# Performance work log

Measured on AMD Instinct MI355X. Metric: run time of the kernel, lower is better.

## Reference

```python
import jax, jax.numpy as jnp
import numpy as np

B, S, D = 2, 2048, 1024
E, K, DFF = 8, 2, 4 * 1024
EPS_GATE = 1e-8
EPS_LN = 1e-5


def setup_inputs() -> dict:
    key = jax.random.key(0)
    ks = jax.random.split(key, 4)
    scaled = lambda k, shape, fan: (jax.random.normal(k, shape, jnp.float32) / np.sqrt(fan).astype(np.float32))
    return {
        "x": jax.random.normal(ks[0], (B, S, D), jnp.float32),
        "Wg": scaled(ks[1], (D, E), D),
        "bg": jnp.zeros((E,), jnp.float32),
        "W1": scaled(ks[2], (E, D, DFF), D),
        "b1": jnp.zeros((E, DFF), jnp.float32),
        "W2": scaled(ks[3], (E, DFF, D), DFF),
        "b2": jnp.zeros((E, D), jnp.float32),
        "gamma": jnp.ones((D,), jnp.float32),
        "beta": jnp.zeros((D,), jnp.float32),
    }


def reference(x, Wg, bg, W1, b1, W2, b2, gamma, beta):
    b, s, d = x.shape
    xf = x.reshape(-1, d)                       # [T, D]
    T = xf.shape[0]
    num_experts = Wg.shape[1]

    # Gating: softmax over experts, top-k, renormalize selected weights.
    logits = xf @ Wg + bg                       # [T, E]
    w = jax.nn.softmax(logits, axis=-1)
    top_w, top_idx = jax.lax.top_k(w, K)        # [T, K]
    top_w = top_w / (top_w.sum(axis=-1, keepdims=True) + EPS_GATE)

    # Dense combine weights: cw[t, e] = renormalized weight if e selected else 0.
    cw = jnp.zeros((T, num_experts), xf.dtype).at[
        jnp.arange(T)[:, None], top_idx].add(top_w)

    # Expert FFNs (loop over small fixed expert count), weighted combine.
    out = jnp.zeros_like(xf)
    for e in range(num_experts):
        h = jax.nn.gelu(xf @ W1[e] + b1[e], approximate=False)  # [T, DFF]
        y = h @ W2[e] + b2[e]                                    # [T, D]
        out = out + cw[:, e:e + 1] * y

    # LayerNorm over the whole combined output (as in the torch module).
    mu = out.mean(axis=-1, keepdims=True)
    var = out.var(axis=-1, keepdims=True)
    out = (out - mu) / jnp.sqrt(var + EPS_LN) * gamma + beta
    return out.reshape(b, s, d)
```

## Files before the change

### kernel.cpp

```cpp
#include <hip/hip_runtime.h>
#include <hip/hip_bf16.h>

#define TOK  4096
#define DIMD 1024
#define NEXP 8
#define DFFN 4096
#define NSLOT   (TOK*2 + NEXP*128)
#define NRB128  ((TOK*2)/128 + NEXP)

typedef __attribute__((ext_vector_type(8))) short bf16x8;
typedef __attribute__((ext_vector_type(4))) float f32x4;

__device__ __forceinline__ unsigned short f2bf(float f){
  unsigned int u = __float_as_uint(f);
  unsigned int r = u + 0x7FFFu + ((u >> 16) & 1u);
  return (unsigned short)(r >> 16);
}

__device__ __forceinline__ float bf2f(unsigned short h){
  unsigned int u = ((unsigned int)h) << 16;
  return __uint_as_float(u);
}

__device__ __forceinline__ void gload_lds16(const void* g, void* l){
  __builtin_amdgcn_global_load_lds(
      (const __attribute__((address_space(1))) unsigned int*)g,
      (__attribute__((address_space(3))) unsigned int*)l, 16, 0, 0);
}

__global__ __launch_bounds__(256) void k_tr(
    const float* __restrict__ W1, unsigned short* __restrict__ w1t,
    const float* __restrict__ W2, unsigned short* __restrict__ w2t)
{
  int bid = blockIdx.x;
  const float* I; unsigned short* O; int R, C, r0, c0;
  if (bid < 2048){
    const int e = bid >> 8, rem = bid & 255;
    R = DIMD; C = DFFN;
    I = W1 + (size_t)e * R * C; O = w1t + (size_t)e * R * C;
    r0 = (rem >> 5) * 128; c0 = (rem & 31) * 128;
  } else {
    bid -= 2048;
    const int e = bid >> 8, rem = bid & 255;
    R = DFFN; C = DIMD;
    I = W2 + (size_t)e * R * C; O = w2t + (size_t)e * R * C;
    r0 = (rem >> 3) * 128; c0 = (rem & 7) * 128;
  }
  __shared__ alignas(16) unsigned short tile[128*128];
  const int tid = threadIdx.x;
  const int qw = tid & 31;
  const int rw = tid >> 5;
  float4 v[16];
  #pragma unroll
  for (int it = 0; it < 16; ++it){
    const int r = it * 8 + rw;
    v[it] = *(const float4*)(I + (size_t)(r0 + r) * C + c0 + qw * 4);
  }
  #pragma unroll
  for (int it = 0; it < 16; ++it){
    const int r = it * 8 + rw;
    ushort4 o;
    o.x = f2bf(v[it].x); o.y = f2bf(v[it].y); o.z = f2bf(v[it].z); o.w = f2bf(v[it].w);
    const int slot = qw ^ ((r >> 2) & 31);
    *(ushort4*)&tile[r * 128 + slot * 4] = o;
  }
  __syncthreads();
  const int p  = tid & 31;
  const int cb = tid >> 5;
  #pragma unroll
  for (int it = 0; it < 4; ++it){
    const int cg = cb * 4 + it;
    const int sl = (cg ^ p) * 4;
    const ushort4 a0 = *(const ushort4*)&tile[(4*p + 0) * 128 + sl];
    const ushort4 a1 = *(const ushort4*)&tile[(4*p + 1) * 128 + sl];
    const ushort4 a2 = *(const ushort4*)&tile[(4*p + 2) * 128 + sl];
    const ushort4 a3 = *(const ushort4*)&tile[(4*p + 3) * 128 + sl];
    ushort4 o;
    o.x = a0.x; o.y = a1.x; o.z = a2.x; o.w = a3.x;
    *(ushort4*)(O + (size_t)(c0 + 4*cg + 0) * R + r0 + 4*p) = o;
    o.x = a0.y; o.y = a1.y; o.z = a2.y; o.w = a3.y;
    *(ushort4*)(O + (size_t)(c0 + 4*cg + 1) * R + r0 + 4*p) = o;
    o.x = a0.z; o.y = a1.z; o.z = a2.z; o.w = a3.z;
    *(ushort4*)(O + (size_t)(c0 + 4*cg + 2) * R + r0 + 4*p) = o;
    o.x = a0.w; o.y = a1.w; o.z = a2.w; o.w = a3.w;
    *(ushort4*)(O + (size_t)(c0 + 4*cg + 3) * R + r0 + 4*p) = o;
  }
}

__global__ __launch_bounds__(256) void k_gate(
    const float* __restrict__ x, const float* __restrict__ Wg,
    const float* __restrict__ bg, int* __restrict__ topidx,
    float* __restrict__ topw, int* __restrict__ pos, int* __restrict__ count,
    unsigned short* __restrict__ xb)
{
  const int gb = blockIdx.x;
  const int wid = threadIdx.x >> 6, lane = threadIdx.x & 63;
  const int t = gb * 4 + wid;
  const float* xr = x + (size_t)t * DIMD;
  unsigned short* xbr = xb + (size_t)t * DIMD;
  float acc[NEXP] = {0.f,0.f,0.f,0.f,0.f,0.f,0.f,0.f};
  #pragma unroll
  for (int j = 0; j < DIMD/64; ++j){
    const int d = j*64 + lane;
    const float xv = xr[d];
    xbr[d] = f2bf(xv);
    const float4 wa = *(const float4*)(Wg + (size_t)d*NEXP);
    const float4 wb = *(const float4*)(Wg + (size_t)d*NEXP + 4);
    acc[0] += xv*wa.x; acc[1] += xv*wa.y; acc[2] += xv*wa.z; acc[3] += xv*wa.w;
    acc[4] += xv*wb.x; acc[5] += xv*wb.y; acc[6] += xv*wb.z; acc[7] += xv*wb.w;
  }
  #pragma unroll
  for (int e = 0; e < NEXP; ++e){
    float v = acc[e];
    #pragma unroll
    for (int o = 32; o > 0; o >>= 1) v += __shfl_xor(v, o);
    acc[e] = v;
  }
  if (lane == 0){
    float lg[NEXP], m = -1e30f;
    #pragma unroll
    for (int e = 0; e < NEXP; ++e){ lg[e] = acc[e] + bg[e]; m = fmaxf(m, lg[e]); }
    float p[NEXP], S = 0.f;
    #pragma unroll
    for (int e = 0; e < NEXP; ++e){ p[e] = expf(lg[e] - m); S += p[e]; }
    int e0 = 0;
    #pragma unroll
    for (int e = 1; e < NEXP; ++e) if (p[e] > p[e0]) e0 = e;
    int e1 = (e0 == 0) ? 1 : 0;
    #pragma unroll
    for (int e = 0; e < NEXP; ++e){
      if (e == e0 || e == e1) continue;
      if (p[e] > p[e1]) e1 = e;
    }
    const float denom = p[e0] + p[e1] + 1e-8f * S;
    const float w0 = p[e0] / denom, w1 = p[e1] / denom;
    const int p0 = atomicAdd(&count[e0], 1);
    const int p1 = atomicAdd(&count[e1], 1);
    topidx[t*2] = e0; topidx[t*2+1] = e1;
    topw[t*2] = w0;   topw[t*2+1] = w1;
    pos[t*2] = p0;    pos[t*2+1] = p1;
  }
}

__global__ __launch_bounds__(256) void k_scatter(
    const int* __restrict__ topidx, const int* __restrict__ pos,
    const int* __restrict__ count, int* __restrict__ slot_of, int* __restrict__ tok_of)
{
  int basee[NEXP]; int bacc = 0;
  #pragma unroll
  for (int q = 0; q < NEXP; ++q){
    basee[q] = bacc << 7;
    bacc += (count[q] + 127) >> 7;
  }
  const int t = blockIdx.x * 256 + threadIdx.x;
  #pragma unroll
  for (int k = 0; k < 2; ++k){
    const int e = topidx[t*2+k];
    const int g = basee[e] + pos[t*2+k];
    slot_of[t*2+k] = g;
    tok_of[g] = t;
  }
}

template<int KD, int KSLICES, int NT, int MODE, int WAVES, int BM, int BN, int MINW>
__global__ __launch_bounds__(WAVES*64, MINW) void k_gemm(
    const unsigned short* __restrict__ A, const unsigned short* __restrict__ Bt,
    const float* __restrict__ bias, const int* __restrict__ tok_of,
    const int* __restrict__ count,
    unsigned short* __restrict__ outH, unsigned short* __restrict__ outY,
    unsigned short* __restrict__ outY1)
{
  const int by = blockIdx.y;
  int e = -1, b0 = 0;
  #pragma unroll
  for (int q = 0; q < NEXP; ++q){
    const int nb = (count[q] + 127) >> 7;
    if (e < 0){ if (by < b0 + nb) e = q; else b0 += nb; }
  }
  if (e < 0) return;
  const int ct = blockIdx.x;
  const int ks = (KSLICES == 1) ? 0 : blockIdx.z;
  constexpr int KSL = KD / KSLICES;
  const int kbase = ks * KSL;
  const int row0 = by * 128;
  constexpr int T   = WAVES * 64;
  constexpr int RA  = BM*8 / T;
  constexpr int RB  = BN*8 / T;
  constexpr int WN  = BN / 64;
  constexpr int WM  = WAVES / WN;
  constexpr int MR  = BM / WM / 16;
  __shared__ alignas(16) unsigned short sA[BM*64];
  __shared__ alignas(16) unsigned short sB[BN*64];
  const int tid = threadIdx.x, wid = tid >> 6, lane = tid & 63;

  const unsigned short* aptr[RA];
  #pragma unroll
  for (int i = 0; i < RA; ++i){
    const int s = i*T + tid;
    const int row = s >> 3;
    const int c = (s & 7) ^ (row & 7);
    size_t arow;
    if (MODE == 1) arow = (size_t)tok_of[row0 + row] * KD;
    else           arow = (size_t)(row0 + row) * KD;
    aptr[i] = A + arow + kbase + c*8;
  }
  const unsigned short* bptr[RB];
  #pragma unroll
  for (int i = 0; i < RB; ++i){
    const int s = i*T + tid;
    const int row = s >> 3;
    const int c = (s & 7) ^ (row & 7);
    bptr[i] = Bt + ((size_t)e*NT + ct*BN + row) * KD + kbase + c*8;
  }

  f32x4 acc[MR][4] = {};
  const int wr = wid / WN, wc = wid % WN;

  int aoff[MR][2], boff[4][2];
  #pragma unroll
  for (int m = 0; m < MR; ++m){
    #pragma unroll
    for (int s = 0; s < 2; ++s){
      const int rowA = wr*(MR*16) + m*16 + (lane & 15);
      aoff[m][s] = rowA*64 + (((s*4) + (lane >> 4)) ^ (rowA & 7))*8;
    }
  }
  #pragma unroll
  for (int n = 0; n < 4; ++n){
    #pragma unroll
    for (int s = 0; s < 2; ++s){
      const int rowB = wc*64 + n*16 + (lane & 15);
      boff[n][s] = rowB*64 + (((s*4) + (lane >> 4)) ^ (rowB & 7))*8;
    }
  }

  for (int k0 = 0; k0 < KSL; k0 += 64){
    #pragma unroll
    for (int i = 0; i < RA; ++i)
      gload_lds16(aptr[i] + k0, &sA[(i*T + tid - lane)*8]);
    #pragma unroll
    for (int i = 0; i < RB; ++i)
      gload_lds16(bptr[i] + k0, &sB[(i*T + tid - lane)*8]);
    __syncthreads();
    #pragma unroll
    for (int s = 0; s < 2; ++s){
      bf16x8 af[MR], bfr[4];
      #pragma unroll
      for (int m = 0; m < MR; ++m) af[m] = *(const bf16x8*)&sA[aoff[m][s]];
      #pragma unroll
      for (int n = 0; n < 4; ++n) bfr[n] = *(const bf16x8*)&sB[boff[n][s]];
      #pragma unroll
      for (int m = 0; m < MR; ++m)
        #pragma unroll
        for (int n = 0; n < 4; ++n)
          acc[m][n] = __builtin_amdgcn_mfma_f32_16x16x32_bf16(af[m], bfr[n], acc[m][n], 0, 0, 0);
    }
    __syncthreads();
  }

  const float* be = bias + (size_t)e * NT;
  unsigned short* outYs = (ks == 0) ? outY : outY1;
  #pragma unroll
  for (int m = 0; m < MR; ++m){
    #pragma unroll
    for (int n = 0; n < 4; ++n){
      #pragma unroll
      for (int j = 0; j < 4; ++j){
        const int rl = wr*(MR*16) + m*16 + ((lane >> 4) << 2) + j;
        const int ng = ct*BN + wc*64 + n*16 + (lane & 15);
        const size_t orow = (size_t)(row0 + rl) * NT + ng;
        if (MODE == 1){
          const float u = acc[m][n][j] + be[ng];
          float y = 0.7978845608028654f * (u + 0.044715f * u * u * u);
          y = fminf(fmaxf(y, -15.f), 15.f);
          const float ex = __expf(2.f * y);
          const float th = (ex - 1.f) / (ex + 1.f);
          outH[orow] = f2bf(0.5f * u * (1.f + th));
        } else {
          outYs[orow] = f2bf(acc[m][n][j] + ((ks == 0) ? be[ng] : 0.f));
        }
      }
    }
  }
}

__global__ __launch_bounds__(256) void k_combine_ln(
    const unsigned short* __restrict__ Ys0, const unsigned short* __restrict__ Ys1,
    const int* __restrict__ slot_of,
    const float* __restrict__ topw, const float* __restrict__ gamma,
    const float* __restrict__ beta, float* __restrict__ out)
{
  const int t = blockIdx.x;
  const int g0 = slot_of[t*2], g1 = slot_of[t*2+1];
  const float w0 = topw[t*2], w1 = topw[t*2+1];
  const int c = threadIdx.x;
  const ushort4 a0 = *(const ushort4*)(Ys0 + (size_t)g0*DIMD + c*4);
  const ushort4 a1 = *(const ushort4*)(Ys1 + (size_t)g0*DIMD + c*4);
  const ushort4 b0 = *(const ushort4*)(Ys0 + (size_t)g1*DIMD + c*4);
  const ushort4 b1 = *(const ushort4*)(Ys1 + (size_t)g1*DIMD + c*4);
  float4 v;
  v.x = w0*(bf2f(a0.x)+bf2f(a1.x)) + w1*(bf2f(b0.x)+bf2f(b1.x));
  v.y = w0*(bf2f(a0.y)+bf2f(a1.y)) + w1*(bf2f(b0.y)+bf2f(b1.y));
  v.z = w0*(bf2f(a0.z)+bf2f(a1.z)) + w1*(bf2f(b0.z)+bf2f(b1.z));
  v.w = w0*(bf2f(a0.w)+bf2f(a1.w)) + w1*(bf2f(b0.w)+bf2f(b1.w));
  float s  = v.x + v.y + v.z + v.w;
  float ss = v.x*v.x + v.y*v.y + v.z*v.z + v.w*v.w;
  #pragma unroll
  for (int o = 32; o > 0; o >>= 1){ s += __shfl_xor(s, o); ss += __shfl_xor(ss, o); }
  __shared__ float red[8];
  const int wid = threadIdx.x >> 6, lane = threadIdx.x & 63;
  if (lane == 0){ red[wid] = s; red[4 + wid] = ss; }
  __syncthreads();
  const float S  = red[0] + red[1] + red[2] + red[3];
  const float SS = red[4] + red[5] + red[6] + red[7];
  const float mu  = S * (1.f/DIMD);
  const float var = SS * (1.f/DIMD) - mu*mu;
  const float inv = rsqrtf(var + 1e-5f);
  const float4 gm = *(const float4*)(gamma + c*4);
  const float4 bt = *(const float4*)(beta + c*4);
  float4 o;
  o.x = (v.x - mu)*inv*gm.x + bt.x;
  o.y = (v.y - mu)*inv*gm.y + bt.y;
  o.z = (v.z - mu)*inv*gm.z + bt.z;
  o.w = (v.w - mu)*inv*gm.w + bt.w;
  *(float4*)(out + (size_t)t*DIMD + c*4) = o;
}

extern "C" void kernel_launch(void* const* d_in, const int* in_sizes, int n_in,
                              void* d_out, int out_size, void* d_ws, size_t ws_size,
                              hipStream_t stream)
{
  const float* x     = (const float*)d_in[0];
  const float* Wg    = (const float*)d_in[1];
  const float* bg    = (const float*)d_in[2];
  const float* W1    = (const float*)d_in[3];
  const float* b1    = (const float*)d_in[4];
  const float* W2    = (const float*)d_in[5];
  const float* b2    = (const float*)d_in[6];
  const float* gamma = (const float*)d_in[7];
  const float* beta  = (const float*)d_in[8];
  float* out = (float*)d_out;

  char* ws = (char*)d_ws;
  size_t off = 0;
  auto alloc = [&](size_t b){ char* p = ws + off; off += (b + 255) & ~(size_t)255; return p; };
  unsigned short* xb  = (unsigned short*)alloc((size_t)TOK*DIMD*2);
  unsigned short* w1t = (unsigned short*)alloc((size_t)NEXP*DFFN*DIMD*2);
  unsigned short* w2t = (unsigned short*)alloc((size_t)NEXP*DIMD*DFFN*2);
  unsigned short* Hs  = (unsigned short*)alloc((size_t)NSLOT*DFFN*2);
  int*   topidx  = (int*)alloc(TOK*2*4);
  float* topw    = (float*)alloc(TOK*2*4);
  int*   pos     = (int*)alloc(TOK*2*4);
  int*   slot_of = (int*)alloc(TOK*2*4);
  int*   tok_of  = (int*)alloc(NSLOT*4);
  int*   count   = (int*)alloc(256);
  unsigned short* Ys0b = (unsigned short*)w1t;
  unsigned short* Ys1b = Ys0b + (size_t)NSLOT*DIMD;

  (void)hipMemsetAsync(count, 0, NEXP*sizeof(int), stream);
  (void)hipMemsetAsync(tok_of, 0, NSLOT*sizeof(int), stream);
  k_tr<<<4096, 256, 0, stream>>>(W1, w1t, W2, w2t);
  k_gate<<<TOK/4, 256, 0, stream>>>(x, Wg, bg, topidx, topw, pos, count, xb);
  k_scatter<<<TOK/256, 256, 0, stream>>>(topidx, pos, count, slot_of, tok_of);
  k_gemm<DIMD, 1, DFFN, 1, 8, 128, 256, 4><<<dim3(DFFN/256, NRB128), 512, 0, stream>>>(
      xb, w1t, b1, tok_of, count, Hs, nullptr, nullptr);
  k_gemm<DFFN, 2, DIMD, 2, 8, 128, 256, 4><<<dim3(DIMD/256, NRB128, 2), 512, 0, stream>>>(
      Hs, w2t, b2, tok_of, count, nullptr, Ys0b, Ys1b);
  k_combine_ln<<<TOK, 256, 0, stream>>>(Ys0b, Ys1b, slot_of, topw, gamma, beta, out);
}
```

Before: 419.4 us.

## Use 256x256 double-buffered GEMM tiles with phased MFMA/load interleaving

Replaces the single-buffered 128x256 grouped expert GEMM with a 256x256 tile kernel that double-buffers A and B in LDS. The main loop is split into eight phases that interleave global-to-LDS loads with MFMA work, using explicit waitcnt, barriers and setprio. Expert row-block padding grows from 128 to 256 slots to match. The intent is to hide global load latency and raise MFMA utilisation per byte loaded. The costs are more padding waste per expert, fewer blocks in the grid, and a large register and LDS footprint that allows only one block per CU.

```diff
diff --git a/kernel.cpp b/kernel.cpp
--- a/kernel.cpp
+++ b/kernel.cpp
@@ -5,8 +5,8 @@
 #define DIMD 1024
 #define NEXP 8
 #define DFFN 4096
-#define NSLOT   (TOK*2 + NEXP*128)
-#define NRB128  ((TOK*2)/128 + NEXP)
+#define NSLOT   (TOK*2 + NEXP*256)
+#define NRB256  ((TOK*2)/256 + NEXP)
 
 typedef __attribute__((ext_vector_type(8))) short bf16x8;
 typedef __attribute__((ext_vector_type(4))) float f32x4;
@@ -149,8 +149,8 @@
   int basee[NEXP]; int bacc = 0;
   #pragma unroll
   for (int q = 0; q < NEXP; ++q){
-    basee[q] = bacc << 7;
-    bacc += (count[q] + 127) >> 7;
+    basee[q] = bacc << 8;
+    bacc += (count[q] + 255) >> 8;
   }
   const int t = blockIdx.x * 256 + threadIdx.x;
   #pragma unroll
@@ -162,111 +162,134 @@
   }
 }
 
-template<int KD, int KSLICES, int NT, int MODE, int WAVES, int BM, int BN, int MINW>
-__global__ __launch_bounds__(WAVES*64, MINW) void k_gemm(
+template<int KD, int KSLICES, int NT, int MODE>
+__global__ __launch_bounds__(512, 1) void k_gemm8(
     const unsigned short* __restrict__ A, const unsigned short* __restrict__ Bt,
     const float* __restrict__ bias, const int* __restrict__ tok_of,
     const int* __restrict__ count,
     unsigned short* __restrict__ outH, unsigned short* __restrict__ outY,
     unsigned short* __restrict__ outY1)
 {
+  constexpr int BM = 256, BN = 256;
+  constexpr int KSL  = KD / KSLICES;
+  constexpr int NTIL = KSL / 64;
+  static_assert(NTIL >= 4 && (NTIL & 1) == 0, "need even >=4 K-tiles");
   const int by = blockIdx.y;
   int e = -1, b0 = 0;
   #pragma unroll
   for (int q = 0; q < NEXP; ++q){
-    const int nb = (count[q] + 127) >> 7;
+    const int nb = (count[q] + 255) >> 8;
     if (e < 0){ if (by < b0 + nb) e = q; else b0 += nb; }
   }
   if (e < 0) return;
   const int ct = blockIdx.x;
   const int ks = (KSLICES == 1) ? 0 : blockIdx.z;
-  constexpr int KSL = KD / KSLICES;
   const int kbase = ks * KSL;
-  const int row0 = by * 128;
-  constexpr int T   = WAVES * 64;
-  constexpr int RA  = BM*8 / T;
-  constexpr int RB  = BN*8 / T;
-  constexpr int WN  = BN / 64;
-  constexpr int WM  = WAVES / WN;
-  constexpr int MR  = BM / WM / 16;
-  __shared__ alignas(16) unsigned short sA[BM*64];
-  __shared__ alignas(16) unsigned short sB[BN*64];
+  const int row0 = by * 256;
+  __shared__ alignas(16) unsigned short sA[2*BM*64];
+  __shared__ alignas(16) unsigned short sB[2*BN*64];
   const int tid = threadIdx.x, wid = tid >> 6, lane = tid & 63;
-
-  const unsigned short* aptr[RA];
-  #pragma unroll
-  for (int i = 0; i < RA; ++i){
-    const int s = i*T + tid;
-    const int row = s >> 3;
-    const int c = (s & 7) ^ (row & 7);
-    size_t arow;
-    if (MODE == 1) arow = (size_t)tok_of[row0 + row] * KD;
-    else           arow = (size_t)(row0 + row) * KD;
-    aptr[i] = A + arow + kbase + c*8;
-  }
-  const unsigned short* bptr[RB];
-  #pragma unroll
-  for (int i = 0; i < RB; ++i){
-    const int s = i*T + tid;
-    const int row = s >> 3;
-    const int c = (s & 7) ^ (row & 7);
-    bptr[i] = Bt + ((size_t)e*NT + ct*BN + row) * KD + kbase + c*8;
-  }
-
-  f32x4 acc[MR][4] = {};
-  const int wr = wid / WN, wc = wid % WN;
-
-  int aoff[MR][2], boff[4][2];
-  #pragma unroll
-  for (int m = 0; m < MR; ++m){
+  const int wr = wid >> 2, wc = wid & 3;
+
+  const unsigned short* aptr[2][2];
+  const unsigned short* bptr[2][2];
+  #pragma unroll
+  for (int h = 0; h < 2; ++h)
+    #pragma unroll
+    for (int i = 0; i < 2; ++i){
+      const int s = i*512 + tid;
+      const int row = h*128 + (s >> 3);
+      const int c = (s & 7) ^ (row & 7);
+      size_t arow = (MODE == 1) ? (size_t)tok_of[row0 + row] * KD
+                                : (size_t)(row0 + row) * KD;
+      aptr[h][i] = A + arow + kbase + c*8;
+      bptr[h][i] = Bt + ((size_t)e*NT + ct*BN + row) * KD + kbase + c*8;
+    }
+  const int ldst = (tid - lane) * 8;
+
+  #define STG_A(BUF,H,TT) do{ \
+    gload_lds16(aptr[H][0] + (TT)*64, &sA[(BUF)*16384 + (H)*8192 + ldst]); \
+    gload_lds16(aptr[H][1] + (TT)*64, &sA[(BUF)*16384 + (H)*8192 + 4096 + ldst]); }while(0)
+  #define STG_B(BUF,H,TT) do{ \
+    gload_lds16(bptr[H][0] + (TT)*64, &sB[(BUF)*16384 + (H)*8192 + ldst]); \
+    gload_lds16(bptr[H][1] + (TT)*64, &sB[(BUF)*16384 + (H)*8192 + 4096 + ldst]); }while(0)
+
+  int aoff[2][2], boff[4][2];
+  #pragma unroll
+  for (int m2 = 0; m2 < 2; ++m2)
     #pragma unroll
     for (int s = 0; s < 2; ++s){
-      const int rowA = wr*(MR*16) + m*16 + (lane & 15);
-      aoff[m][s] = rowA*64 + (((s*4) + (lane >> 4)) ^ (rowA & 7))*8;
-    }
-  }
-  #pragma unroll
-  for (int n = 0; n < 4; ++n){
+      const int rowA = wr*128 + m2*16 + (lane & 15);
+      aoff[m2][s] = rowA*64 + (((s*4) + (lane >> 4)) ^ (rowA & 7))*8;
+    }
+  #pragma unroll
+  for (int n = 0; n < 4; ++n)
     #pragma unroll
     for (int s = 0; s < 2; ++s){
       const int rowB = wc*64 + n*16 + (lane & 15);
       boff[n][s] = rowB*64 + (((s*4) + (lane >> 4)) ^ (rowB & 7))*8;
     }
-  }
-
-  for (int k0 = 0; k0 < KSL; k0 += 64){
-    #pragma unroll
-    for (int i = 0; i < RA; ++i)
-      gload_lds16(aptr[i] + k0, &sA[(i*T + tid - lane)*8]);
-    #pragma unroll
-    for (int i = 0; i < RB; ++i)
-      gload_lds16(bptr[i] + k0, &sB[(i*T + tid - lane)*8]);
-    __syncthreads();
-    #pragma unroll
-    for (int s = 0; s < 2; ++s){
-      bf16x8 af[MR], bfr[4];
-      #pragma unroll
-      for (int m = 0; m < MR; ++m) af[m] = *(const bf16x8*)&sA[aoff[m][s]];
-      #pragma unroll
-      for (int n = 0; n < 4; ++n) bfr[n] = *(const bf16x8*)&sB[boff[n][s]];
-      #pragma unroll
-      for (int m = 0; m < MR; ++m)
-        #pragma unroll
-        for (int n = 0; n < 4; ++n)
-          acc[m][n] = __builtin_amdgcn_mfma_f32_16x16x32_bf16(af[m], bfr[n], acc[m][n], 0, 0, 0);
-    }
-    __syncthreads();
-  }
+
+  f32x4 acc[8][4] = {};
+  bf16x8 bfr[4][2];
+
+  STG_B(0,0,0); STG_B(0,1,0); STG_A(0,0,0); STG_A(0,1,0);
+  STG_B(1,0,1); STG_B(1,1,1); STG_A(1,0,1);
+  asm volatile("s_waitcnt vmcnt(6)" ::: "memory");
+  __builtin_amdgcn_sched_barrier(0);
+  __builtin_amdgcn_s_barrier();
+
+  #define PHASE(BUF, MQ, BLOAD, PSTMT, DOVM) { \
+    if (BLOAD){ \
+      _Pragma("unroll") for (int n = 0; n < 4; ++n) \
+        _Pragma("unroll") for (int s = 0; s < 2; ++s) \
+          bfr[n][s] = *(const bf16x8*)&sB[(BUF)*16384 + boff[n][s]]; \
+    } \
+    bf16x8 af[2][2]; \
+    _Pragma("unroll") for (int m2 = 0; m2 < 2; ++m2) \
+      _Pragma("unroll") for (int s = 0; s < 2; ++s) \
+        af[m2][s] = *(const bf16x8*)&sA[(BUF)*16384 + (MQ)*2048 + aoff[m2][s]]; \
+    PSTMT; \
+    __builtin_amdgcn_s_barrier(); \
+    asm volatile("s_waitcnt lgkmcnt(0)" ::: "memory"); \
+    __builtin_amdgcn_sched_barrier(0); \
+    __builtin_amdgcn_s_setprio(1); \
+    _Pragma("unroll") for (int m2 = 0; m2 < 2; ++m2) \
+      _Pragma("unroll") for (int n = 0; n < 4; ++n) \
+        _Pragma("unroll") for (int s = 0; s < 2; ++s) \
+          acc[(MQ)*2+m2][n] = __builtin_amdgcn_mfma_f32_16x16x32_bf16( \
+              af[m2][s], bfr[n][s], acc[(MQ)*2+m2][n], 0, 0, 0); \
+    __builtin_amdgcn_s_setprio(0); \
+    if (DOVM){ asm volatile("s_waitcnt vmcnt(6)" ::: "memory"); } \
+    __builtin_amdgcn_s_barrier(); \
+  }
+
+  for (int it = 0; it < NTIL/2; ++it){
+    const int t1 = 2*it + 1;
+    const int t2 = (2*it + 2) % NTIL;
+    const int t3 = (2*it + 3) % NTIL;
+    PHASE(0, 0, 1, STG_A(1,1,t1), 0)
+    PHASE(0, 1, 0, STG_B(0,0,t2), 0)
+    PHASE(0, 2, 0, STG_B(0,1,t2), 0)
+    PHASE(0, 3, 0, STG_A(0,0,t2), 1)
+    PHASE(1, 0, 1, STG_A(0,1,t2), 0)
+    PHASE(1, 1, 0, STG_B(1,0,t3), 0)
+    PHASE(1, 2, 0, STG_B(1,1,t3), 0)
+    PHASE(1, 3, 0, STG_A(1,0,t3), 1)
+  }
+  #undef PHASE
+  #undef STG_A
+  #undef STG_B
 
   const float* be = bias + (size_t)e * NT;
   unsigned short* outYs = (ks == 0) ? outY : outY1;
   #pragma unroll
-  for (int m = 0; m < MR; ++m){
+  for (int m = 0; m < 8; ++m){
     #pragma unroll
     for (int n = 0; n < 4; ++n){
       #pragma unroll
       for (int j = 0; j < 4; ++j){
-        const int rl = wr*(MR*16) + m*16 + ((lane >> 4) << 2) + j;
+        const int rl = wr*128 + m*16 + ((lane >> 4) << 2) + j;
         const int ng = ct*BN + wc*64 + n*16 + (lane & 15);
         const size_t orow = (size_t)(row0 + rl) * NT + ng;
         if (MODE == 1){
@@ -362,9 +385,9 @@
   k_tr<<<4096, 256, 0, stream>>>(W1, w1t, W2, w2t);
   k_gate<<<TOK/4, 256, 0, stream>>>(x, Wg, bg, topidx, topw, pos, count, xb);
   k_scatter<<<TOK/256, 256, 0, stream>>>(topidx, pos, count, slot_of, tok_of);
-  k_gemm<DIMD, 1, DFFN, 1, 8, 128, 256, 4><<<dim3(DFFN/256, NRB128), 512, 0, stream>>>(
+  k_gemm8<DIMD, 1, DFFN, 1><<<dim3(DFFN/256, NRB256), 512, 0, stream>>>(
       xb, w1t, b1, tok_of, count, Hs, nullptr, nullptr);
-  k_gemm<DFFN, 2, DIMD, 2, 8, 128, 256, 4><<<dim3(DIMD/256, NRB128, 2), 512, 0, stream>>>(
+  k_gemm8<DFFN, 2, DIMD, 2><<<dim3(DIMD/256, NRB256, 2), 512, 0, stream>>>(
       Hs, w2t, b2, tok_of, count, nullptr, Ys0b, Ys1b);
   k_combine_ln<<<TOK, 256, 0, stream>>>(Ys0b, Ys1b, slot_of, topw, gamma, beta, out);
 }
```

New measurement: 449.2 us. 7.1% more time.
